# Performance work log

Hardware: AMD Instinct MI355X
Metric: run time of the kernel (lower is better)

## Reference

```python
import jax, jax.numpy as jnp
import numpy as np

B, L, C, H, K, P, NB = 32, 512, 512, 512, 16, 96, 4  # enc_in == hidden_size required by MlpBlockTimesteps
EPS = 1e-5


def setup_inputs() -> dict:
    key = jax.random.key(0)
    ks = jax.random.split(key, 12)
    g = lambda i, shape, s=0.02: jax.random.normal(ks[i], shape, jnp.float32) * s
    return {
        'x': jax.random.normal(ks[0], (B, L, C), jnp.float32),
        'rev_w': jnp.ones((C,), jnp.float32), 'rev_b': jnp.zeros((C,), jnp.float32),
        'mlp_w1': g(1, (L, H)), 'mlp_b1': jnp.zeros((H,), jnp.float32),
        'mlp_w2': g(2, (H, H)), 'mlp_b2': jnp.zeros((H,), jnp.float32),
        'cluster_embeds': jax.random.normal(ks[3], (K, H), jnp.float32),
        'wq': g(4, (H, H)), 'bq': jnp.zeros((H,), jnp.float32),
        'wk': g(5, (H, H)), 'bk': jnp.zeros((H,), jnp.float32),
        'wv': g(6, (H, H)), 'bv': jnp.zeros((H,), jnp.float32),
        'ts_ln_g': jnp.ones((C,), jnp.float32), 'ts_ln_b': jnp.zeros((C,), jnp.float32),
        'ts_w': g(7, (C, C)), 'ts_b': jnp.zeros((C,), jnp.float32),
        'ch_ln_g': jnp.ones((C,), jnp.float32), 'ch_ln_b': jnp.zeros((C,), jnp.float32),
        'ch_w1': g(8, (C, H)), 'ch_b1': jnp.zeros((H,), jnp.float32),
        'ch_w2': g(9, (H, C)), 'ch_b2': jnp.zeros((C,), jnp.float32),
        'out_w': g(10, (C, H, P)), 'out_b': jnp.zeros((C, P), jnp.float32),
    }


def _ln(z, g, b):
    m = z.mean(-1, keepdims=True)
    v = jnp.mean((z - m) ** 2, axis=-1, keepdims=True)
    return (z - m) / jnp.sqrt(v + EPS) * g + b


def _gelu(z):
    return jax.nn.gelu(z, approximate=False)


def _forward(x, rev_w, rev_b, mlp_w1, mlp_b1, mlp_w2, mlp_b2, cluster_embeds,
             wq, bq, wk, bk, wv, bv, ts_ln_g, ts_ln_b, ts_w, ts_b,
             ch_ln_g, ch_ln_b, ch_w1, ch_b1, ch_w2, ch_b2, out_w, out_b):
    # RevIN norm (stats over time dim=1)
    mean = x.mean(axis=1, keepdims=True)                      # [B,1,C]
    std = jnp.sqrt(jnp.var(x, axis=1, keepdims=True) + EPS)
    xn = (x - mean) / std * rev_w + rev_b                      # [B,L,C]
    xt = xn.transpose(0, 2, 1)                                 # [B,C,L]
    # channel MLP: Linear(L->H) -> ReLU -> Linear(H->H)
    h = jnp.maximum(xt @ mlp_w1 + mlp_b1, 0.0) @ mlp_w2 + mlp_b2  # [B,C,H]
    # cosine-sim soft routing + bernoulli hard mask
    cn = cluster_embeds / jnp.maximum(jnp.linalg.norm(cluster_embeds, axis=-1, keepdims=True), 1e-12)
    hn = h / jnp.maximum(jnp.linalg.norm(h, axis=-1, keepdims=True), 1e-12)
    p = jax.nn.softmax(hn @ cn.T, axis=-1)                     # [B,C,K]
    M = jax.random.bernoulli(jax.random.key(42), p).astype(h.dtype)
    # masked exp-attention over clusters
    Q = cluster_embeds @ wq + bq                               # [K,H]
    Kk = h @ wk + bk                                           # [B,C,H]
    V = h @ wv + bv
    scores = jnp.einsum('kh,bch->bkc', Q, Kk) / jnp.sqrt(jnp.float32(H))
    am = jnp.exp(scores) * M.transpose(0, 2, 1)                # [B,K,C]
    aw = am / am.sum(-1, keepdims=True)
    Cc = jnp.einsum('bkc,bch->bkh', aw, V)                     # [B,K,H]
    ce_new = jax.lax.stop_gradient(Cc.mean(0))                 # mimics .data.copy_ (no grad into C)
    # mixer block, NB iterations with shared weights (enc_in == hidden_size)
    Hm = h
    for _ in range(NB):
        z = Hm.transpose(0, 2, 1)                              # [B,H,C]
        Hm = (z + _gelu(_ln(z, ts_ln_g, ts_ln_b) @ ts_w + ts_b)).transpose(0, 2, 1)
        z = Hm.transpose(0, 2, 1)                              # [B,H,C]
        y2 = _gelu(_ln(z, ch_ln_g, ch_ln_b) @ ch_w1 + ch_b1) @ ch_w2 + ch_b2
        Hm = (z + y2).transpose(0, 2, 1)                       # [B,C,H]
    # per-channel expert projections gated by theta (uses UPDATED cluster embeds)
    theta = jnp.einsum('bck,kh->bch', p, ce_new)               # [B,C,H]
    y = jnp.einsum('bch,chp->bcp', Hm * theta, out_w) + out_b  # [B,C,P]
    y = y.transpose(0, 2, 1)                                   # [B,P,C]
    # RevIN denorm
    y = (y - rev_b) / (rev_w + EPS * EPS)
    return y * std + mean


def reference(x, rev_w, rev_b, mlp_w1, mlp_b1, mlp_w2, mlp_b2, cluster_embeds,
              wq, bq, wk, bk, wv, bv, ts_ln_g, ts_ln_b, ts_w, ts_b,
              ch_ln_g, ch_ln_b, ch_w1, ch_b1, ch_w2, ch_b2, out_w, out_b):
    return _forward(x, rev_w, rev_b, mlp_w1, mlp_b1, mlp_w2, mlp_b2, cluster_embeds,
                    wq, bq, wk, bk, wv, bv, ts_ln_g, ts_ln_b, ts_w, ts_b,
                    ch_ln_g, ch_ln_b, ch_w1, ch_b1, ch_w2, ch_b2, out_w, out_b)
```

## Files before the change

### kernel.cpp

```cpp
#include <hip/hip_runtime.h>
#include <math.h>

#define B_  32
#define L_  512
#define C_  512
#define H_  512
#define K_  16
#define P_  96
#define NB_ 4

typedef unsigned short u16;
typedef __attribute__((ext_vector_type(8))) __bf16 bf16x8;
typedef __attribute__((ext_vector_type(4))) float f32x4;


__device__ __forceinline__ float gelu_f(float x) {
    return 0.5f * x * (1.0f + erff(x * 0.70710678118654752440f));
}

__device__ __forceinline__ u16 f2bf(float f) {
    union { float f; unsigned u; } v; v.f = f;
    unsigned r = v.u + 0x7fffu + ((v.u >> 16) & 1u);
    return (u16)(r >> 16);
}
__device__ __forceinline__ float bf2f(u16 h) {
    union { unsigned u; float f; } v; v.u = ((unsigned)h) << 16;
    return v.f;
}

__device__ __forceinline__ void block_sum2_256(float& a, float& b) {
    __shared__ float la[4], lb[4];
    #pragma unroll
    for (int off = 32; off; off >>= 1) {
        a += __shfl_down(a, off);
        b += __shfl_down(b, off);
    }
    int wid = threadIdx.x >> 6;
    if ((threadIdx.x & 63) == 0) { la[wid] = a; lb[wid] = b; }
    __syncthreads();
    a = la[0] + la[1] + la[2] + la[3];
    b = lb[0] + lb[1] + lb[2] + lb[3];
}

__device__ __forceinline__ void threefry2x32(unsigned k0, unsigned k1,
                                             unsigned& x0, unsigned& x1) {
    const unsigned ks0 = k0, ks1 = k1, ks2 = k0 ^ k1 ^ 0x1BD11BDAu;
    x0 += ks0; x1 += ks1;
#define TF_ROT(v, r) (((v) << (r)) | ((v) >> (32 - (r))))
#define TF_R(r) { x0 += x1; x1 = TF_ROT(x1, r); x1 ^= x0; }
    TF_R(13) TF_R(15) TF_R(26) TF_R(6)   x0 += ks1; x1 += ks2 + 1u;
    TF_R(17) TF_R(29) TF_R(16) TF_R(24)  x0 += ks2; x1 += ks0 + 2u;
    TF_R(13) TF_R(15) TF_R(26) TF_R(6)   x0 += ks0; x1 += ks1 + 3u;
    TF_R(17) TF_R(29) TF_R(16) TF_R(24)  x0 += ks1; x1 += ks2 + 4u;
    TF_R(13) TF_R(15) TF_R(26) TF_R(6)   x0 += ks2; x1 += ks0 + 5u;
#undef TF_R
#undef TF_ROT
}

#define GLL16(g, l) __builtin_amdgcn_global_load_lds( \
    (const __attribute__((address_space(1))) void*)(g), \
    (__attribute__((address_space(3))) void*)(l), 16, 0, 0)


__global__ __launch_bounds__(256) void revin_stats(const float* __restrict__ x,
                                                   float* __restrict__ meanB,
                                                   float* __restrict__ stdB) {
    int b = blockIdx.x;
    int c = blockIdx.y * 256 + threadIdx.x;
    const float* xp = x + (size_t)b * L_ * C_ + c;
    float s = 0.f, ss = 0.f;
    for (int l = 0; l < L_; ++l) {
        float v = xp[(size_t)l * C_];
        s += v; ss += v * v;
    }
    float m = s * (1.0f / L_);
    float var = ss * (1.0f / L_) - m * m;
    meanB[b * C_ + c] = m;
    stdB[b * C_ + c]  = sqrtf(var + 1e-5f);
}

__global__ __launch_bounds__(256) void transpose_revin(const float* __restrict__ x,
                                                       const float* __restrict__ meanB,
                                                       const float* __restrict__ stdB,
                                                       const float* __restrict__ rw,
                                                       const float* __restrict__ rb,
                                                       u16* __restrict__ xt) {
    __shared__ float tile[32][33];
    int b = blockIdx.x, l0 = blockIdx.y * 32, c0 = blockIdx.z * 32;
    int tx = threadIdx.x, ty = threadIdx.y;
    for (int i = ty; i < 32; i += 8) {
        int l = l0 + i, c = c0 + tx;
        float v = x[((size_t)b * L_ + l) * C_ + c];
        v = (v - meanB[b * C_ + c]) / stdB[b * C_ + c] * rw[c] + rb[c];
        tile[i][tx] = v;
    }
    __syncthreads();
    for (int i = ty; i < 32; i += 8) {
        int c = c0 + i, l = l0 + tx;
        xt[((size_t)b * C_ + c) * L_ + l] = f2bf(tile[tx][i]);
    }
}

__global__ __launch_bounds__(256) void transpose_b(const float* __restrict__ in,
                                                   float* __restrict__ out) {
    __shared__ float tile[32][33];
    int b = blockIdx.x, r0 = blockIdx.y * 32, c0 = blockIdx.z * 32;
    int tx = threadIdx.x, ty = threadIdx.y;
    for (int i = ty; i < 32; i += 8)
        tile[i][tx] = in[((size_t)b * 512 + r0 + i) * 512 + c0 + tx];
    __syncthreads();
    for (int i = ty; i < 32; i += 8)
        out[((size_t)b * 512 + c0 + i) * 512 + r0 + tx] = tile[tx][i];
}

struct WPtrs { const float* src[7]; u16* dst[7]; };
__global__ __launch_bounds__(256) void convert_w(WPtrs wp) {
    __shared__ float tile[32][33];
    int wi = blockIdx.z;
    const float* src = wp.src[wi];
    u16* dst = wp.dst[wi];
    int r0 = blockIdx.y * 32, c0 = blockIdx.x * 32;
    int tx = threadIdx.x, ty = threadIdx.y;
    for (int i = ty; i < 32; i += 8)
        tile[i][tx] = src[(size_t)(r0 + i) * 512 + c0 + tx];
    __syncthreads();
    for (int i = ty; i < 32; i += 8)
        dst[(size_t)(c0 + i) * 512 + r0 + tx] = f2bf(tile[tx][i]);
}

template <int EPI>
__global__ __launch_bounds__(256) void gemm_bf16(const u16* __restrict__ A,
                                                 const u16* __restrict__ Bt,
                                                 const float* __restrict__ bias,
                                                 float* __restrict__ C32,
                                                 u16* __restrict__ C16,
                                                 int M, int N, int K) {
    __shared__ u16 As[128 * 32];
    __shared__ u16 Bs[128 * 32];
    int tid = threadIdx.x;
    int m0 = blockIdx.y * 128, n0 = blockIdx.x * 128;
    int lane = tid & 63, wave = tid >> 6;
    int wm = wave >> 1, wn = wave & 1;
    int col = lane & 15, quad = lane >> 4;
    int koff = quad * 8;

    int qa0 = tid, qa1 = tid + 256;
    const u16* Ag0 = A + (size_t)(m0 + (qa0 >> 2)) * K + (qa0 & 3) * 8;
    const u16* Ag1 = A + (size_t)(m0 + (qa1 >> 2)) * K + (qa1 & 3) * 8;
    const u16* Bg0 = Bt + (size_t)(n0 + (qa0 >> 2)) * K + (qa0 & 3) * 8;
    const u16* Bg1 = Bt + (size_t)(n0 + (qa1 >> 2)) * K + (qa1 & 3) * 8;
    u16* Al0 = &As[qa0 * 8];
    u16* Al1 = &As[qa1 * 8];
    u16* Bl0 = &Bs[qa0 * 8];
    u16* Bl1 = &Bs[qa1 * 8];

    f32x4 acc[4][4];
    #pragma unroll
    for (int i = 0; i < 4; ++i)
        #pragma unroll
        for (int j = 0; j < 4; ++j)
            acc[i][j] = (f32x4){0.f, 0.f, 0.f, 0.f};

    for (int k0 = 0; k0 < K; k0 += 32) {
        GLL16(Ag0 + k0, Al0);
        GLL16(Ag1 + k0, Al1);
        GLL16(Bg0 + k0, Bl0);
        GLL16(Bg1 + k0, Bl1);
        __syncthreads();
        bf16x8 af[4], bfr[4];
        #pragma unroll
        for (int mt = 0; mt < 4; ++mt)
            af[mt] = *(const bf16x8*)&As[(wm * 64 + mt * 16 + col) * 32 + koff];
        #pragma unroll
        for (int nt = 0; nt < 4; ++nt)
            bfr[nt] = *(const bf16x8*)&Bs[(wn * 64 + nt * 16 + col) * 32 + koff];
        #pragma unroll
        for (int mt = 0; mt < 4; ++mt)
            #pragma unroll
            for (int nt = 0; nt < 4; ++nt)
                acc[mt][nt] = __builtin_amdgcn_mfma_f32_16x16x32_bf16(
                    af[mt], bfr[nt], acc[mt][nt], 0, 0, 0);
        __syncthreads();
    }

    float bb[4];
    #pragma unroll
    for (int nt = 0; nt < 4; ++nt) bb[nt] = bias[n0 + wn * 64 + nt * 16 + col];
    #pragma unroll
    for (int mt = 0; mt < 4; ++mt) {
        int mbase = m0 + wm * 64 + mt * 16 + quad * 4;
        #pragma unroll
        for (int r = 0; r < 4; ++r) {
            size_t rowoff = (size_t)(mbase + r) * N;
            #pragma unroll
            for (int nt = 0; nt < 4; ++nt) {
                int gn = n0 + wn * 64 + nt * 16 + col;
                float t = acc[mt][nt][r] + bb[nt];
                if (EPI == 1) t = fmaxf(t, 0.f);
                if (EPI == 0) {
                    C32[rowoff + gn] = t;
                } else if (EPI == 1 || EPI == 6) {
                    C16[rowoff + gn] = f2bf(t);
                } else if (EPI == 5) {
                    C32[rowoff + gn] = t;
                    C16[rowoff + gn] = f2bf(t);
                }
            }
        }
    }
}

__global__ __launch_bounds__(256) void gemm_f32(const float* __restrict__ A,
                                                const float* __restrict__ Bm,
                                                const float* __restrict__ bias,
                                                float* __restrict__ Cm,
                                                int M, int N, int K) {
    __shared__ float As[16][64];
    __shared__ float Bs[16][64];
    int tid = threadIdx.x;
    int tx = tid & 15, ty = tid >> 4;
    int m0 = blockIdx.y * 64, n0 = blockIdx.x * 64;
    float acc[4][4] = {};
    for (int k0 = 0; k0 < K; k0 += 16) {
        {
            int r = tid >> 2, cc = (tid & 3) * 4, gm = m0 + r;
            float4 v = make_float4(0.f, 0.f, 0.f, 0.f);
            if (gm < M) v = *(const float4*)(A + (size_t)gm * K + k0 + cc);
            As[cc + 0][r] = v.x; As[cc + 1][r] = v.y;
            As[cc + 2][r] = v.z; As[cc + 3][r] = v.w;
        }
        {
            int r = tid >> 4, cc = (tid & 15) * 4;
            *(float4*)&Bs[r][cc] = *(const float4*)(Bm + (size_t)(k0 + r) * N + n0 + cc);
        }
        __syncthreads();
        #pragma unroll
        for (int kk = 0; kk < 16; ++kk) {
            float4 a4 = *(const float4*)&As[kk][ty * 4];
            float4 b4 = *(const float4*)&Bs[kk][tx * 4];
            float av[4] = {a4.x, a4.y, a4.z, a4.w};
            float bv[4] = {b4.x, b4.y, b4.z, b4.w};
            #pragma unroll
            for (int i = 0; i < 4; ++i)
                #pragma unroll
                for (int j = 0; j < 4; ++j)
                    acc[i][j] += av[i] * bv[j];
        }
        __syncthreads();
    }
    int gn = n0 + tx * 4;
    float4 b4 = *(const float4*)(bias + gn);
    float bb[4] = {b4.x, b4.y, b4.z, b4.w};
    #pragma unroll
    for (int i = 0; i < 4; ++i) {
        int gm = m0 + ty * 4 + i;
        if (gm >= M) break;
        float* cp = Cm + (size_t)gm * N + gn;
        *(float4*)cp = make_float4(acc[i][0] + bb[0], acc[i][1] + bb[1],
                                   acc[i][2] + bb[2], acc[i][3] + bb[3]);
    }
}

__global__ __launch_bounds__(256) void normalize_rows16(const float* __restrict__ ce,
                                                        float* __restrict__ cn) {
    int k = blockIdx.x, tid = threadIdx.x;
    float2 v = ((const float2*)(ce + (size_t)k * 512))[tid];
    float ss = v.x * v.x + v.y * v.y, dummy = 0.f;
    block_sum2_256(ss, dummy);
    float inv = 1.0f / fmaxf(sqrtf(ss), 1e-12f);
    float2 o; o.x = v.x * inv; o.y = v.y * inv;
    ((float2*)(cn + (size_t)k * 512))[tid] = o;
}

__global__ __launch_bounds__(256) void routing_kernel(const float* __restrict__ h,
                                                      const float* __restrict__ cn,
                                                      float* __restrict__ p) {
    int tid = threadIdx.x;
    int r = tid >> 4, k = tid & 15;
    int row = blockIdx.x * 16 + r;
    const float4* hp = (const float4*)(h + (size_t)row * 512);
    const float4* ck = (const float4*)(cn + (size_t)k * 512);
    float ss = 0.f;
    #pragma unroll
    for (int j = k * 8; j < k * 8 + 8; ++j) {
        float4 v = hp[j];
        ss += v.x * v.x + v.y * v.y + v.z * v.z + v.w * v.w;
    }
    #pragma unroll
    for (int off = 8; off; off >>= 1) ss += __shfl_xor(ss, off, 16);
    float inv = 1.0f / fmaxf(sqrtf(ss), 1e-12f);
    float d = 0.f;
    for (int j = 0; j < 128; ++j) {
        float4 a = hp[j], b = ck[j];
        d += a.x * b.x + a.y * b.y + a.z * b.z + a.w * b.w;
    }
    d *= inv;
    float mx = d;
    #pragma unroll
    for (int off = 8; off; off >>= 1) mx = fmaxf(mx, __shfl_xor(mx, off, 16));
    float e = expf(d - mx);
    float s = e;
    #pragma unroll
    for (int off = 8; off; off >>= 1) s += __shfl_xor(s, off, 16);
    p[(size_t)row * 16 + k] = e / s;
}

__global__ __launch_bounds__(256) void attn_scores(const float* __restrict__ Kk,
                                                   const float* __restrict__ Q,
                                                   const float* __restrict__ pbuf,
                                                   float* __restrict__ am) {
    int tid = threadIdx.x;
    int k = tid >> 4, r = tid & 15;
    int row = blockIdx.x * 16 + r;
    int b = row >> 9, c = row & 511;
    const float4* kp = (const float4*)(Kk + (size_t)row * 512);
    const float4* qp = (const float4*)(Q + (size_t)k * 512);
    float d = 0.f;
    for (int j = 0; j < 128; ++j) {
        float4 a = kp[j], q = qp[j];
        d += a.x * q.x + a.y * q.y + a.z * q.z + a.w * q.w;
    }
    d *= 0.044194173824159216f;
    int j = row * 16 + k;
    const int HALF = (B_ * C_ * K_) / 2;
    unsigned x0 = (j < HALF) ? (unsigned)j : (unsigned)(j - HALF);
    unsigned x1 = x0 + (unsigned)HALF;
    threefry2x32(0u, 42u, x0, x1);
    unsigned bits = (j < HALF) ? x0 : x1;
    float u = __uint_as_float((bits >> 9) | 0x3f800000u) - 1.0f;
    float m = (u < pbuf[j]) ? 1.0f : 0.0f;
    am[((size_t)b * 16 + k) * 512 + c] = expf(d) * m;
}

__global__ __launch_bounds__(256) void row_recip(const float* __restrict__ am,
                                                 float* __restrict__ recip) {
    int rk = blockIdx.x, tid = threadIdx.x;
    float2 v = ((const float2*)(am + (size_t)rk * 512))[tid];
    float s = v.x + v.y, dummy = 0.f;
    block_sum2_256(s, dummy);
    if (tid == 0) recip[rk] = 1.0f / s;
}

__global__ __launch_bounds__(256) void cc_partial(const float* __restrict__ am,
                                                  const float* __restrict__ recip,
                                                  const u16* __restrict__ V16,
                                                  float* __restrict__ Ccp) {
    int b = blockIdx.x, cs = blockIdx.y;
    int c0 = cs * 64, tid = threadIdx.x;
    __shared__ float awS[16 * 64];
    for (int idx = tid; idx < 1024; idx += 256) {
        int k = idx >> 6, cj = idx & 63;
        awS[idx] = am[((size_t)b * 16 + k) * 512 + c0 + cj] * recip[b * 16 + k];
    }
    __syncthreads();
    float acc0[16] = {}, acc1[16] = {};
    for (int cj = 0; cj < 64; ++cj) {
        const u16* vp = V16 + ((size_t)(b * 512) + c0 + cj) * 512;
        unsigned pk = ((const unsigned*)vp)[tid];
        float v0 = bf2f((u16)(pk & 0xffffu));
        float v1 = bf2f((u16)(pk >> 16));
        #pragma unroll
        for (int k = 0; k < 16; ++k) {
            float a = awS[k * 64 + cj];
            acc0[k] += a * v0;
            acc1[k] += a * v1;
        }
    }
    float* out = Ccp + ((size_t)(b * 8 + cs)) * 8192;
    #pragma unroll
    for (int k = 0; k < 16; ++k) {
        float2 o; o.x = acc0[k]; o.y = acc1[k];
        ((float2*)(out + k * 512))[tid] = o;
    }
}

__global__ __launch_bounds__(256) void cc_mean(const float* __restrict__ Ccp,
                                               float* __restrict__ ce) {
    int idx = blockIdx.x * 256 + threadIdx.x;
    float s = 0.f;
    for (int sl = 0; sl < 256; ++sl) s += Ccp[(size_t)sl * 8192 + idx];
    ce[idx] = s * (1.0f / B_);
}

__global__ __launch_bounds__(256) void mixer_fused(
    float* __restrict__ z,
    const u16* __restrict__ tsw, const u16* __restrict__ chw1,
    const u16* __restrict__ chw2,
    const float* __restrict__ tslng, const float* __restrict__ tslnb,
    const float* __restrict__ tsb,
    const float* __restrict__ chlng, const float* __restrict__ chlnb,
    const float* __restrict__ chb1, const float* __restrict__ chb2) {
    __shared__ u16 A16[32 * 520];
    __shared__ float statS[32 * 2];
    __shared__ float partS[4 * 32 * 2];
    __shared__ float vecS[7 * 512];

    int tid = threadIdx.x, lane = tid & 63, wave = tid >> 6;
    int col = lane & 15, quad = lane >> 4;
    int m0 = blockIdx.x * 32;

    {
        const float* vsrc[7] = {tslng, tslnb, tsb, chlng, chlnb, chb1, chb2};
        for (int i = tid; i < 7 * 512; i += 256) vecS[i] = vsrc[i >> 9][i & 511];
    }

    f32x4 zr[16];
    float* zbase = z + (size_t)m0 * 512;
    #pragma unroll
    for (int mt = 0; mt < 2; ++mt)
        #pragma unroll
        for (int nt = 0; nt < 8; ++nt)
            #pragma unroll
            for (int r = 0; r < 4; ++r)
                zr[mt * 8 + nt][r] =
                    zbase[(size_t)(mt * 16 + quad * 4 + r) * 512 +
                          wave * 128 + nt * 16 + col];

    auto stats = [&]() {
        #pragma unroll
        for (int mt = 0; mt < 2; ++mt)
            #pragma unroll
            for (int r = 0; r < 4; ++r) {
                float s = 0.f, ss = 0.f;
                #pragma unroll
                for (int nt = 0; nt < 8; ++nt) {
                    float v = zr[mt * 8 + nt][r];
                    s += v; ss += v * v;
                }
                #pragma unroll
                for (int o = 8; o; o >>= 1) {
                    s += __shfl_xor(s, o, 16);
                    ss += __shfl_xor(ss, o, 16);
                }
                if (col == 0) {
                    int m = mt * 16 + quad * 4 + r;
                    partS[(wave * 32 + m) * 2 + 0] = s;
                    partS[(wave * 32 + m) * 2 + 1] = ss;
                }
            }
        __syncthreads();
        if (tid < 32) {
            float s = 0.f, ss = 0.f;
            #pragma unroll
            for (int w = 0; w < 4; ++w) {
                s += partS[(w * 32 + tid) * 2];
                ss += partS[(w * 32 + tid) * 2 + 1];
            }
            float mean = s * (1.0f / 512.0f);
            float var = ss * (1.0f / 512.0f) - mean * mean;
            statS[tid * 2] = mean;
            statS[tid * 2 + 1] = rsqrtf(var + 1e-5f);
        }
        __syncthreads();
    };

    auto writeNorm = [&](int gi, int bi) {
        float mn[8], rs[8];
        #pragma unroll
        for (int mt = 0; mt < 2; ++mt)
            #pragma unroll
            for (int r = 0; r < 4; ++r) {
                int m = mt * 16 + quad * 4 + r;
                mn[mt * 4 + r] = statS[m * 2];
                rs[mt * 4 + r] = statS[m * 2 + 1];
            }
        #pragma unroll
        for (int nt = 0; nt < 8; ++nt) {
            int n = wave * 128 + nt * 16 + col;
            float g = vecS[gi * 512 + n], bb = vecS[bi * 512 + n];
            #pragma unroll
            for (int mt = 0; mt < 2; ++mt)
                #pragma unroll
                for (int r = 0; r < 4; ++r) {
                    int m = mt * 16 + quad * 4 + r;
                    float v = (zr[mt * 8 + nt][r] - mn[mt * 4 + r]) *
                              rs[mt * 4 + r] * g + bb;
                    A16[m * 520 + n] = f2bf(v);
                }
        }
        __syncthreads();
    };

    f32x4 acc[16];
    auto gemm = [&](const u16* __restrict__ W) {
        #pragma unroll
        for (int i = 0; i < 16; ++i) acc[i] = (f32x4){0.f, 0.f, 0.f, 0.f};
        #pragma unroll 4
        for (int kc = 0; kc < 16; ++kc) {
            bf16x8 a0 = *(const bf16x8*)&A16[col * 520 + kc * 32 + quad * 8];
            bf16x8 a1 = *(const bf16x8*)&A16[(16 + col) * 520 + kc * 32 + quad * 8];
            #pragma unroll
            for (int nt = 0; nt < 8; ++nt) {
                bf16x8 bf = *(const bf16x8*)
                    &W[(size_t)(wave * 128 + nt * 16 + col) * 512 + kc * 32 + quad * 8];
                acc[nt] = __builtin_amdgcn_mfma_f32_16x16x32_bf16(a0, bf, acc[nt], 0, 0, 0);
                acc[8 + nt] = __builtin_amdgcn_mfma_f32_16x16x32_bf16(a1, bf, acc[8 + nt], 0, 0, 0);
            }
        }
    };

    for (int it = 0; it < NB_; ++it) {
        stats();
        writeNorm(0, 1);
        gemm(tsw);
        #pragma unroll
        for (int nt = 0; nt < 8; ++nt) {
            float bb = vecS[2 * 512 + wave * 128 + nt * 16 + col];
            #pragma unroll
            for (int mt = 0; mt < 2; ++mt)
                #pragma unroll
                for (int r = 0; r < 4; ++r)
                    zr[mt * 8 + nt][r] += gelu_f(acc[mt * 8 + nt][r] + bb);
        }
        stats();
        writeNorm(3, 4);
        gemm(chw1);
        __syncthreads();
        #pragma unroll
        for (int nt = 0; nt < 8; ++nt) {
            int n = wave * 128 + nt * 16 + col;
            float bb = vecS[5 * 512 + n];
            #pragma unroll
            for (int mt = 0; mt < 2; ++mt)
                #pragma unroll
                for (int r = 0; r < 4; ++r) {
                    int m = mt * 16 + quad * 4 + r;
                    A16[m * 520 + n] = f2bf(gelu_f(acc[mt * 8 + nt][r] + bb));
                }
        }
        __syncthreads();
        gemm(chw2);
        #pragma unroll
        for (int nt = 0; nt < 8; ++nt) {
            float bb = vecS[6 * 512 + wave * 128 + nt * 16 + col];
            #pragma unroll
            for (int mt = 0; mt < 2; ++mt)
                #pragma unroll
                for (int r = 0; r < 4; ++r)
                    zr[mt * 8 + nt][r] += acc[mt * 8 + nt][r] + bb;
        }
    }

    #pragma unroll
    for (int mt = 0; mt < 2; ++mt)
        #pragma unroll
        for (int nt = 0; nt < 8; ++nt)
            #pragma unroll
            for (int r = 0; r < 4; ++r)
                zbase[(size_t)(mt * 16 + quad * 4 + r) * 512 +
                      wave * 128 + nt * 16 + col] = zr[mt * 8 + nt][r];
}

__global__ __launch_bounds__(256) void outproj_mfma(
    const float* __restrict__ Hm, const float* __restrict__ pbuf,
    const float* __restrict__ ce, const float* __restrict__ out_w,
    const float* __restrict__ out_b, const float* __restrict__ rev_w,
    const float* __restrict__ rev_b, const float* __restrict__ meanB,
    const float* __restrict__ stdB, float* __restrict__ out) {
    __shared__ float pS[32 * 16];
    __shared__ u16 A16[32 * 520];
    __shared__ u16 Bs[4][96 * 40];
    __shared__ float redS[4][32 * 96];

    int c = blockIdx.x, tid = threadIdx.x;
    int lane = tid & 63, wave = tid >> 6;
    int col = lane & 15, quad = lane >> 4;

    for (int idx = tid; idx < 512; idx += 256) {
        int b = idx >> 4, k = idx & 15;
        pS[idx] = pbuf[((size_t)(b * 512 + c)) * 16 + k];
    }
    __syncthreads();

    {
        int h0 = lane * 8;
        f32x4 th[8][2];
        #pragma unroll
        for (int b = 0; b < 8; ++b) {
            th[b][0] = (f32x4){0.f, 0.f, 0.f, 0.f};
            th[b][1] = (f32x4){0.f, 0.f, 0.f, 0.f};
        }
        for (int k = 0; k < 16; ++k) {
            f32x4 ce0 = *(const f32x4*)&ce[k * 512 + h0];
            f32x4 ce1 = *(const f32x4*)&ce[k * 512 + h0 + 4];
            #pragma unroll
            for (int b = 0; b < 8; ++b) {
                float pk = pS[(wave * 8 + b) * 16 + k];
                th[b][0] += ce0 * pk;
                th[b][1] += ce1 * pk;
            }
        }
        #pragma unroll
        for (int b = 0; b < 8; ++b) {
            int bb = wave * 8 + b;
            const f32x4* hp = (const f32x4*)&Hm[((size_t)(bb * 512 + c)) * 512 + h0];
            f32x4 g0 = hp[0] * th[b][0];
            f32x4 g1 = hp[1] * th[b][1];
            ushort4 o0, o1;
            o0.x = f2bf(g0[0]); o0.y = f2bf(g0[1]); o0.z = f2bf(g0[2]); o0.w = f2bf(g0[3]);
            o1.x = f2bf(g1[0]); o1.y = f2bf(g1[1]); o1.z = f2bf(g1[2]); o1.w = f2bf(g1[3]);
            *(ushort4*)&A16[bb * 520 + h0] = o0;
            *(ushort4*)&A16[bb * 520 + h0 + 4] = o1;
        }
    }
    __syncthreads();

    f32x4 pacc[12];
    #pragma unroll
    for (int i = 0; i < 12; ++i) pacc[i] = (f32x4){0.f, 0.f, 0.f, 0.f};
    const size_t wbase = (size_t)c * 512 * 96;
    for (int i = 0; i < 4; ++i) {
        int kc = wave * 4 + i;
        {
            const float4* wsrc = (const float4*)(out_w + wbase + (size_t)kc * 32 * 96);
            #pragma unroll
            for (int t = 0; t < 12; ++t) {
                int flat4 = lane + t * 64;
                float4 v = wsrc[flat4];
                int kk = flat4 / 24, p4 = (flat4 % 24) * 4;
                Bs[wave][(p4 + 0) * 40 + kk] = f2bf(v.x);
                Bs[wave][(p4 + 1) * 40 + kk] = f2bf(v.y);
                Bs[wave][(p4 + 2) * 40 + kk] = f2bf(v.z);
                Bs[wave][(p4 + 3) * 40 + kk] = f2bf(v.w);
            }
        }
        __syncthreads();
        #pragma unroll
        for (int mt = 0; mt < 2; ++mt) {
            bf16x8 a = *(const bf16x8*)&A16[(mt * 16 + col) * 520 + kc * 32 + quad * 8];
            #pragma unroll
            for (int nt = 0; nt < 6; ++nt) {
                bf16x8 bf = *(const bf16x8*)&Bs[wave][(nt * 16 + col) * 40 + quad * 8];
                pacc[mt * 6 + nt] = __builtin_amdgcn_mfma_f32_16x16x32_bf16(
                    a, bf, pacc[mt * 6 + nt], 0, 0, 0);
            }
        }
        __syncthreads();
    }
    #pragma unroll
    for (int mt = 0; mt < 2; ++mt)
        #pragma unroll
        for (int nt = 0; nt < 6; ++nt)
            #pragma unroll
            for (int r = 0; r < 4; ++r) {
                int b = mt * 16 + quad * 4 + r;
                int p = nt * 16 + col;
                redS[wave][b * 96 + p] = pacc[mt * 6 + nt][r];
            }
    __syncthreads();

    float inv_rw = 1.0f / (rev_w[c] + 1e-10f);
    float rb = rev_b[c];
    for (int e = tid; e < 3072; e += 256) {
        float v = redS[0][e] + redS[1][e] + redS[2][e] + redS[3][e];
        int b = e / 96, p = e - b * 96;
        v += out_b[(size_t)c * 96 + p];
        float y = (v - rb) * inv_rw * stdB[b * 512 + c] + meanB[b * 512 + c];
        out[((size_t)b * 96 + p) * 512 + c] = y;
    }
}


extern "C" void kernel_launch(void* const* d_in, const int* in_sizes, int n_in,
                              void* d_out, int out_size, void* d_ws, size_t ws_size,
                              hipStream_t stream) {
    const float* x        = (const float*)d_in[0];
    const float* rev_w    = (const float*)d_in[1];
    const float* rev_b    = (const float*)d_in[2];
    const float* mlp_w1   = (const float*)d_in[3];
    const float* mlp_b1   = (const float*)d_in[4];
    const float* mlp_w2   = (const float*)d_in[5];
    const float* mlp_b2   = (const float*)d_in[6];
    const float* clu_emb  = (const float*)d_in[7];
    const float* wq       = (const float*)d_in[8];
    const float* bq       = (const float*)d_in[9];
    const float* wk       = (const float*)d_in[10];
    const float* bk       = (const float*)d_in[11];
    const float* wv       = (const float*)d_in[12];
    const float* bv       = (const float*)d_in[13];
    const float* ts_ln_g  = (const float*)d_in[14];
    const float* ts_ln_b  = (const float*)d_in[15];
    const float* ts_w     = (const float*)d_in[16];
    const float* ts_b     = (const float*)d_in[17];
    const float* ch_ln_g  = (const float*)d_in[18];
    const float* ch_ln_b  = (const float*)d_in[19];
    const float* ch_w1    = (const float*)d_in[20];
    const float* ch_b1    = (const float*)d_in[21];
    const float* ch_w2    = (const float*)d_in[22];
    const float* ch_b2    = (const float*)d_in[23];
    const float* out_w    = (const float*)d_in[24];
    const float* out_b    = (const float*)d_in[25];

    float* f = (float*)d_ws;
    const size_t SLOT = (size_t)(B_ * C_) * H_;
    float* F0 = f;
    float* F1 = f + SLOT;
    u16*  X16 = (u16*)(f + 2 * SLOT);
    u16*  T16 = (u16*)(f + 2 * SLOT + SLOT / 2);
    float* sm = f + 3 * SLOT;
    u16* Wt[7];
    for (int i = 0; i < 7; ++i) { Wt[i] = (u16*)sm; sm += 131072; }
    float* meanB  = sm; sm += B_ * C_;
    float* stdB   = sm; sm += B_ * C_;
    float* pbuf   = sm; sm += B_ * C_ * K_;
    float* ambuf  = sm; sm += B_ * K_ * C_;
    float* recips = sm; sm += B_ * K_;
    float* cebuf  = sm; sm += K_ * H_;
    float* cnbuf  = sm; sm += K_ * H_;
    float* Qbuf   = sm; sm += K_ * H_;
    float* Ccp = F1;

    dim3 ggrid(4, 128);
    dim3 t_grid(B_, 16, 16);
    dim3 t_blk(32, 8);
    const int Mrows = B_ * C_;

    revin_stats<<<dim3(B_, 2), 256, 0, stream>>>(x, meanB, stdB);
    transpose_revin<<<t_grid, t_blk, 0, stream>>>(x, meanB, stdB, rev_w, rev_b, X16);
    WPtrs wp;
    wp.src[0] = mlp_w1; wp.src[1] = mlp_w2; wp.src[2] = wk; wp.src[3] = wv;
    wp.src[4] = ts_w;   wp.src[5] = ch_w1;  wp.src[6] = ch_w2;
    for (int i = 0; i < 7; ++i) wp.dst[i] = Wt[i];
    convert_w<<<dim3(16, 16, 7), t_blk, 0, stream>>>(wp);
    gemm_f32<<<dim3(8, 1), 256, 0, stream>>>(clu_emb, wq, bq, Qbuf, K_, H_, H_);
    gemm_bf16<1><<<ggrid, 256, 0, stream>>>(X16, Wt[0], mlp_b1, nullptr, T16,
                                            Mrows, H_, L_);
    gemm_bf16<5><<<ggrid, 256, 0, stream>>>(T16, Wt[1], mlp_b2, F0, X16,
                                            Mrows, H_, H_);
    normalize_rows16<<<K_, 256, 0, stream>>>(clu_emb, cnbuf);
    routing_kernel<<<Mrows / 16, 256, 0, stream>>>(F0, cnbuf, pbuf);
    gemm_bf16<0><<<ggrid, 256, 0, stream>>>(X16, Wt[2], bk, F1, nullptr,
                                            Mrows, H_, H_);
    gemm_bf16<6><<<ggrid, 256, 0, stream>>>(X16, Wt[3], bv, nullptr, T16,
                                            Mrows, H_, H_);
    attn_scores<<<Mrows / 16, 256, 0, stream>>>(F1, Qbuf, pbuf, ambuf);
    row_recip<<<B_ * K_, 256, 0, stream>>>(ambuf, recips);
    cc_partial<<<dim3(B_, 8), 256, 0, stream>>>(ambuf, recips, T16, Ccp);
    cc_mean<<<(K_ * H_) / 256, 256, 0, stream>>>(Ccp, cebuf);
    transpose_b<<<t_grid, t_blk, 0, stream>>>(F0, F1);
    mixer_fused<<<Mrows / 32, 256, 0, stream>>>(F1, Wt[4], Wt[5], Wt[6],
                                                ts_ln_g, ts_ln_b, ts_b,
                                                ch_ln_g, ch_ln_b, ch_b1, ch_b2);
    transpose_b<<<t_grid, t_blk, 0, stream>>>(F1, F0);
    outproj_mfma<<<C_, 256, 0, stream>>>(F0, pbuf, cebuf, out_w, out_b,
                                         rev_w, rev_b, meanB, stdB,
                                         (float*)d_out);
}
```

Measured before the change: 1.170 ms.

## Split fused mixer work across eight waves per block to halve register footprint

The fused mixer kernel now launches 512 threads (8 waves) per 32-row block instead of 256, so each wave owns 64 output columns rather than 128. That halves the per-thread accumulator and residual register arrays, and launch_bounds(512,4) asks the compiler for higher occupancy. The GEMM inner loop now issues all four B-fragment global loads before the MFMAs to expose more memory parallelism. In exchange, the cross-wave LayerNorm reduction has more partials to combine, and a barrier is added at the end of each iteration.

```diff
diff --git a/kernel.cpp b/kernel.cpp
--- a/kernel.cpp
+++ b/kernel.cpp
@@ -382,7 +382,7 @@
     ce[idx] = s * (1.0f / B_);
 }
 
-__global__ __launch_bounds__(256) void mixer_fused(
+__global__ __launch_bounds__(512, 4) void mixer_fused2(
     float* __restrict__ z,
     const u16* __restrict__ tsw, const u16* __restrict__ chw1,
     const u16* __restrict__ chw2,
@@ -391,30 +391,30 @@
     const float* __restrict__ chlng, const float* __restrict__ chlnb,
     const float* __restrict__ chb1, const float* __restrict__ chb2) {
     __shared__ u16 A16[32 * 520];
+    __shared__ float vecS[7 * 512];
+    __shared__ float partS[8 * 32 * 2];
     __shared__ float statS[32 * 2];
-    __shared__ float partS[4 * 32 * 2];
-    __shared__ float vecS[7 * 512];
-
-    int tid = threadIdx.x, lane = tid & 63, wave = tid >> 6;
+
+    int tid = threadIdx.x, lane = tid & 63, w = tid >> 6;
     int col = lane & 15, quad = lane >> 4;
     int m0 = blockIdx.x * 32;
+    int nb = w * 64 + col;
 
     {
         const float* vsrc[7] = {tslng, tslnb, tsb, chlng, chlnb, chb1, chb2};
-        for (int i = tid; i < 7 * 512; i += 256) vecS[i] = vsrc[i >> 9][i & 511];
-    }
-
-    f32x4 zr[16];
+        for (int i = tid; i < 7 * 512; i += 512) vecS[i] = vsrc[i >> 9][i & 511];
+    }
+
+    f32x4 zr[8];
     float* zbase = z + (size_t)m0 * 512;
     #pragma unroll
     for (int mt = 0; mt < 2; ++mt)
         #pragma unroll
-        for (int nt = 0; nt < 8; ++nt)
+        for (int nt = 0; nt < 4; ++nt)
             #pragma unroll
             for (int r = 0; r < 4; ++r)
-                zr[mt * 8 + nt][r] =
-                    zbase[(size_t)(mt * 16 + quad * 4 + r) * 512 +
-                          wave * 128 + nt * 16 + col];
+                zr[mt * 4 + nt][r] =
+                    zbase[(size_t)(mt * 16 + quad * 4 + r) * 512 + nb + nt * 16];
 
     auto stats = [&]() {
         #pragma unroll
@@ -423,8 +423,8 @@
             for (int r = 0; r < 4; ++r) {
                 float s = 0.f, ss = 0.f;
                 #pragma unroll
-                for (int nt = 0; nt < 8; ++nt) {
-                    float v = zr[mt * 8 + nt][r];
+                for (int nt = 0; nt < 4; ++nt) {
+                    float v = zr[mt * 4 + nt][r];
                     s += v; ss += v * v;
                 }
                 #pragma unroll
@@ -434,17 +434,17 @@
                 }
                 if (col == 0) {
                     int m = mt * 16 + quad * 4 + r;
-                    partS[(wave * 32 + m) * 2 + 0] = s;
-                    partS[(wave * 32 + m) * 2 + 1] = ss;
+                    partS[(w * 32 + m) * 2 + 0] = s;
+                    partS[(w * 32 + m) * 2 + 1] = ss;
                 }
             }
         __syncthreads();
         if (tid < 32) {
             float s = 0.f, ss = 0.f;
             #pragma unroll
-            for (int w = 0; w < 4; ++w) {
-                s += partS[(w * 32 + tid) * 2];
-                ss += partS[(w * 32 + tid) * 2 + 1];
+            for (int wv = 0; wv < 8; ++wv) {
+                s += partS[(wv * 32 + tid) * 2];
+                ss += partS[(wv * 32 + tid) * 2 + 1];
             }
             float mean = s * (1.0f / 512.0f);
             float var = ss * (1.0f / 512.0f) - mean * mean;
@@ -455,47 +455,44 @@
     };
 
     auto writeNorm = [&](int gi, int bi) {
-        float mn[8], rs[8];
-        #pragma unroll
-        for (int mt = 0; mt < 2; ++mt)
-            #pragma unroll
-            for (int r = 0; r < 4; ++r) {
-                int m = mt * 16 + quad * 4 + r;
-                mn[mt * 4 + r] = statS[m * 2];
-                rs[mt * 4 + r] = statS[m * 2 + 1];
-            }
-        #pragma unroll
-        for (int nt = 0; nt < 8; ++nt) {
-            int n = wave * 128 + nt * 16 + col;
+        #pragma unroll
+        for (int nt = 0; nt < 4; ++nt) {
+            int n = nb + nt * 16;
             float g = vecS[gi * 512 + n], bb = vecS[bi * 512 + n];
             #pragma unroll
             for (int mt = 0; mt < 2; ++mt)
                 #pragma unroll
                 for (int r = 0; r < 4; ++r) {
                     int m = mt * 16 + quad * 4 + r;
-                    float v = (zr[mt * 8 + nt][r] - mn[mt * 4 + r]) *
-                              rs[mt * 4 + r] * g + bb;
+                    float v = (zr[mt * 4 + nt][r] - statS[m * 2]) *
+                              statS[m * 2 + 1] * g + bb;
                     A16[m * 520 + n] = f2bf(v);
                 }
         }
         __syncthreads();
     };
 
-    f32x4 acc[16];
+    f32x4 acc[8];
     auto gemm = [&](const u16* __restrict__ W) {
         #pragma unroll
-        for (int i = 0; i < 16; ++i) acc[i] = (f32x4){0.f, 0.f, 0.f, 0.f};
+        for (int i = 0; i < 8; ++i) acc[i] = (f32x4){0.f, 0.f, 0.f, 0.f};
+        const u16* wb = W + (size_t)nb * 512 + quad * 8;
         #pragma unroll 4
         for (int kc = 0; kc < 16; ++kc) {
+            bf16x8 b0 = *(const bf16x8*)&wb[kc * 32];
+            bf16x8 b1 = *(const bf16x8*)&wb[16 * 512 + kc * 32];
+            bf16x8 b2 = *(const bf16x8*)&wb[32 * 512 + kc * 32];
+            bf16x8 b3 = *(const bf16x8*)&wb[48 * 512 + kc * 32];
             bf16x8 a0 = *(const bf16x8*)&A16[col * 520 + kc * 32 + quad * 8];
             bf16x8 a1 = *(const bf16x8*)&A16[(16 + col) * 520 + kc * 32 + quad * 8];
-            #pragma unroll
-            for (int nt = 0; nt < 8; ++nt) {
-                bf16x8 bf = *(const bf16x8*)
-                    &W[(size_t)(wave * 128 + nt * 16 + col) * 512 + kc * 32 + quad * 8];
-                acc[nt] = __builtin_amdgcn_mfma_f32_16x16x32_bf16(a0, bf, acc[nt], 0, 0, 0);
-                acc[8 + nt] = __builtin_amdgcn_mfma_f32_16x16x32_bf16(a1, bf, acc[8 + nt], 0, 0, 0);
-            }
+            acc[0] = __builtin_amdgcn_mfma_f32_16x16x32_bf16(a0, b0, acc[0], 0, 0, 0);
+            acc[1] = __builtin_amdgcn_mfma_f32_16x16x32_bf16(a0, b1, acc[1], 0, 0, 0);
+            acc[2] = __builtin_amdgcn_mfma_f32_16x16x32_bf16(a0, b2, acc[2], 0, 0, 0);
+            acc[3] = __builtin_amdgcn_mfma_f32_16x16x32_bf16(a0, b3, acc[3], 0, 0, 0);
+            acc[4] = __builtin_amdgcn_mfma_f32_16x16x32_bf16(a1, b0, acc[4], 0, 0, 0);
+            acc[5] = __builtin_amdgcn_mfma_f32_16x16x32_bf16(a1, b1, acc[5], 0, 0, 0);
+            acc[6] = __builtin_amdgcn_mfma_f32_16x16x32_bf16(a1, b2, acc[6], 0, 0, 0);
+            acc[7] = __builtin_amdgcn_mfma_f32_16x16x32_bf16(a1, b3, acc[7], 0, 0, 0);
         }
     };
 
@@ -504,51 +501,52 @@
         writeNorm(0, 1);
         gemm(tsw);
         #pragma unroll
-        for (int nt = 0; nt < 8; ++nt) {
-            float bb = vecS[2 * 512 + wave * 128 + nt * 16 + col];
+        for (int nt = 0; nt < 4; ++nt) {
+            float bb = vecS[2 * 512 + nb + nt * 16];
             #pragma unroll
             for (int mt = 0; mt < 2; ++mt)
                 #pragma unroll
                 for (int r = 0; r < 4; ++r)
-                    zr[mt * 8 + nt][r] += gelu_f(acc[mt * 8 + nt][r] + bb);
+                    zr[mt * 4 + nt][r] += gelu_f(acc[mt * 4 + nt][r] + bb);
         }
         stats();
         writeNorm(3, 4);
         gemm(chw1);
         __syncthreads();
         #pragma unroll
-        for (int nt = 0; nt < 8; ++nt) {
-            int n = wave * 128 + nt * 16 + col;
+        for (int nt = 0; nt < 4; ++nt) {
+            int n = nb + nt * 16;
             float bb = vecS[5 * 512 + n];
             #pragma unroll
             for (int mt = 0; mt < 2; ++mt)
                 #pragma unroll
                 for (int r = 0; r < 4; ++r) {
                     int m = mt * 16 + quad * 4 + r;
-                    A16[m * 520 + n] = f2bf(gelu_f(acc[mt * 8 + nt][r] + bb));
+                    A16[m * 520 + n] = f2bf(gelu_f(acc[mt * 4 + nt][r] + bb));
                 }
         }
         __syncthreads();
         gemm(chw2);
         #pragma unroll
-        for (int nt = 0; nt < 8; ++nt) {
-            float bb = vecS[6 * 512 + wave * 128 + nt * 16 + col];
+        for (int nt = 0; nt < 4; ++nt) {
+            float bb = vecS[6 * 512 + nb + nt * 16];
             #pragma unroll
             for (int mt = 0; mt < 2; ++mt)
                 #pragma unroll
                 for (int r = 0; r < 4; ++r)
-                    zr[mt * 8 + nt][r] += acc[mt * 8 + nt][r] + bb;
-        }
+                    zr[mt * 4 + nt][r] += acc[mt * 4 + nt][r] + bb;
+        }
+        __syncthreads();
     }
 
     #pragma unroll
     for (int mt = 0; mt < 2; ++mt)
         #pragma unroll
-        for (int nt = 0; nt < 8; ++nt)
+        for (int nt = 0; nt < 4; ++nt)
             #pragma unroll
             for (int r = 0; r < 4; ++r)
-                zbase[(size_t)(mt * 16 + quad * 4 + r) * 512 +
-                      wave * 128 + nt * 16 + col] = zr[mt * 8 + nt][r];
+                zbase[(size_t)(mt * 16 + quad * 4 + r) * 512 + nb + nt * 16] =
+                    zr[mt * 4 + nt][r];
 }
 
 __global__ __launch_bounds__(256) void outproj_mfma(
@@ -738,9 +736,9 @@
     cc_partial<<<dim3(B_, 8), 256, 0, stream>>>(ambuf, recips, T16, Ccp);
     cc_mean<<<(K_ * H_) / 256, 256, 0, stream>>>(Ccp, cebuf);
     transpose_b<<<t_grid, t_blk, 0, stream>>>(F0, F1);
-    mixer_fused<<<Mrows / 32, 256, 0, stream>>>(F1, Wt[4], Wt[5], Wt[6],
-                                                ts_ln_g, ts_ln_b, ts_b,
-                                                ch_ln_g, ch_ln_b, ch_b1, ch_b2);
+    mixer_fused2<<<Mrows / 32, 512, 0, stream>>>(F1, Wt[4], Wt[5], Wt[6],
+                                                 ts_ln_g, ts_ln_b, ts_b,
+                                                 ch_ln_g, ch_ln_b, ch_b1, ch_b2);
     transpose_b<<<t_grid, t_blk, 0, stream>>>(F1, F0);
     outproj_mfma<<<C_, 256, 0, stream>>>(F0, pbuf, cebuf, out_w, out_b,
                                          rev_w, rev_b, meanB, stdB,
```

After: 1.001 ms. 14.4% less time.
